# Performance work log

Hardware: AMD Instinct MI355X
Metric: run time of the kernel (lower is better)

Reference implementation:

```python
import jax, jax.numpy as jnp
import numpy as np

A, B, D = 64, 128, 256   # batch, route nodes, feature_dim
H, C = 64, 32            # hidden_capsule, center_num
NUM_ITERS = 3


def _squash(t, axis=-1):
    sq = jnp.sum(t * t, axis=axis, keepdims=True)
    return (sq / (1.0 + sq)) * t / jnp.sqrt(sq)


def _route(priors, n_iters):
    # priors: [K, A, R, D]; dynamic routing over axis=2 (R).
    # Original keeps logits of priors' full shape, but they stay constant
    # along D (init zeros, delta has keepdim on last axis), so [K,A,R,1]
    # is exactly equivalent and avoids a redundant [K,A,R,D] buffer.
    logits = jnp.zeros(priors.shape[:-1] + (1,), priors.dtype)
    outputs = None
    for i in range(n_iters):
        probs = jax.nn.softmax(logits, axis=2)          # [K,A,R,1]
        outputs = _squash(jnp.sum(probs * priors, axis=2, keepdims=True))  # [K,A,1,D]
        if i != n_iters - 1:
            logits = logits + jnp.sum(priors * outputs, axis=-1, keepdims=True)
    return outputs


def setup_inputs() -> dict:
    key = jax.random.key(0)
    k1, k2, k3 = jax.random.split(key, 3)
    x = jax.random.normal(k1, (A, B, D), dtype=jnp.float32)
    route_weights1 = jax.random.normal(k2, (H, D, D), dtype=jnp.float32)
    route_weights = jax.random.normal(k3, (C, D, D), dtype=jnp.float32)
    return {"x": x, "route_weights1": route_weights1, "route_weights": route_weights}


def reference(x, route_weights1, route_weights):
    # stage 1: priors1[h,a,b,:] = x[a,b,:] @ W1[h]  -> [H,A,B,D]
    priors1 = jnp.einsum('abd,hde->habe', x, route_weights1)
    out1 = _route(priors1, NUM_ITERS)                  # [H,A,1,D]
    out1 = jnp.transpose(out1[:, :, 0, :], (1, 0, 2))  # squeeze + transpose(0,1) -> [A,H,D]
    # stage 2: priors[c,a,h,:] = out1[a,h,:] @ W[c]   -> [C,A,H,D]
    priors = jnp.einsum('ahd,cde->cahe', out1, route_weights)
    out = _route(priors, NUM_ITERS)                    # [C,A,1,D]
    return out[:, :, 0, :]                             # squeeze -> [C,A,D]
```

## Files before the change

kernel.cpp:

```cpp
#include <hip/hip_runtime.h>
#include <hip/hip_bf16.h>

typedef __attribute__((ext_vector_type(8))) short bf16x8;
typedef __attribute__((ext_vector_type(4))) float f32x4;
typedef unsigned short u16;
typedef unsigned int u32;

__device__ __forceinline__ u32 bf16_rne(float f) {
  u32 u = __float_as_uint(f);
  return (u + 0x7FFFu + ((u >> 16) & 1u)) >> 16;
}
__device__ __forceinline__ float bf16_val(u32 b) { return __uint_as_float(b << 16); }

__device__ __forceinline__ void g2l16(const u16* g, u16* l) {
  __builtin_amdgcn_global_load_lds(
      (const __attribute__((address_space(1))) u32*)g,
      (__attribute__((address_space(3))) u32*)l, 16, 0, 0);
}

__global__ void split_arr(const float* __restrict__ in,
                          u16* __restrict__ hi, u16* __restrict__ lo, int n4) {
  int i = blockIdx.x * 256 + threadIdx.x;
  if (i >= n4) return;
  float4 v = ((const float4*)in)[i];
  u32 h0 = bf16_rne(v.x), h1 = bf16_rne(v.y), h2 = bf16_rne(v.z), h3 = bf16_rne(v.w);
  u32 l0 = bf16_rne(v.x - bf16_val(h0));
  u32 l1 = bf16_rne(v.y - bf16_val(h1));
  u32 l2 = bf16_rne(v.z - bf16_val(h2));
  u32 l3 = bf16_rne(v.w - bf16_val(h3));
  ushort4 hv; hv.x = (u16)h0; hv.y = (u16)h1; hv.z = (u16)h2; hv.w = (u16)h3;
  ushort4 lv; lv.x = (u16)l0; lv.y = (u16)l1; lv.z = (u16)l2; lv.w = (u16)l3;
  ((ushort4*)hi)[i] = hv;
  ((ushort4*)lo)[i] = lv;
}

__global__ void split_transpose256(const float* __restrict__ in,
                                   u16* __restrict__ hi, u16* __restrict__ lo) {
  __shared__ float tile[32][33];
  const size_t off = (size_t)blockIdx.z * 65536;
  const int tx = threadIdx.x, ty = threadIdx.y;
#pragma unroll
  for (int i = 0; i < 4; ++i) {
    int y = blockIdx.y * 32 + ty + i * 8;
    int x = blockIdx.x * 32 + tx;
    tile[ty + i * 8][tx] = in[off + (size_t)y * 256 + x];
  }
  __syncthreads();
#pragma unroll
  for (int i = 0; i < 4; ++i) {
    float v = tile[tx][ty + i * 8];
    u32 hb = bf16_rne(v);
    u32 lb = bf16_rne(v - bf16_val(hb));
    size_t idx = off + (size_t)(blockIdx.x * 32 + ty + i * 8) * 256 + blockIdx.y * 32 + tx;
    hi[idx] = (u16)hb;
    lo[idx] = (u16)lb;
  }
}

template <int R>
__global__ __launch_bounds__(512, 4) void caps_route(
    const u16* __restrict__ Ahi_g,
    const u16* __restrict__ Alo_g,
    const u16* __restrict__ Whi,
    const u16* __restrict__ Wlo,
    u16* __restrict__ o1hi, u16* __restrict__ o1lo,
    float* __restrict__ outp,
    int KN, int stage) {
  constexpr int MTW = R / 32;
  constexpr int NA = R / 16;
  constexpr int NTOT = 2 * NA + 32;
  __shared__ u16 BUF[NTOT * 512];
  __shared__ __align__(16) float smat[2][256];
  __shared__ __align__(16) float wlog[4][R];
  __shared__ float logits[R];
  __shared__ __align__(16) float probs[R];
  __shared__ float sqpart[4];

  u16* Ahi = BUF;
  u16* Alo = BUF + NA * 512;
  u16* Bhi = BUF + 2 * NA * 512;
  u16* Blo = BUF + 2 * NA * 512 + 8192;

  const int tid = threadIdx.x;
  const int w = tid >> 6, lane = tid & 63, q = lane >> 4, li = lane & 15;
  const int mg = w >> 2, eg = w & 3;
  const int kk = blockIdx.x >> 6;
  const int a  = blockIdx.x & 63;

  const u16* ArH = Ahi_g + (size_t)a * R * 256;
  const u16* ArL = Alo_g + (size_t)a * R * 256;
  const u16* WhR = Whi + (size_t)kk * 65536;
  const u16* WlR = Wlo + (size_t)kk * 65536;

  f32x4 acc[MTW][4] = {};

  const int sub = lane >> 2, p = lane & 3;
  const int laneoff = sub * 256 + p * 8;

  for (int ks = 0; ks < 8; ++ks) {
    const int k0 = ks * 32;
#pragma unroll
    for (int c = w; c < NTOT; c += 8) {
      const u16* g;
      if (c < NA)              g = ArH + (c) * 4096;
      else if (c < 2 * NA)     g = ArL + (c - NA) * 4096;
      else if (c < 2 * NA + 16) g = WhR + (c - 2 * NA) * 4096;
      else                     g = WlR + (c - 2 * NA - 16) * 4096;
      g2l16(g + laneoff + k0, BUF + c * 512 + lane * 8);
    }
    __syncthreads();
    bf16x8 bh[4], bl[4];
#pragma unroll
    for (int ct = 0; ct < 4; ++ct) {
      int e = eg * 64 + ct * 16 + li;
      bh[ct] = *(const bf16x8*)(Bhi + e * 32 + q * 8);
      bl[ct] = *(const bf16x8*)(Blo + e * 32 + q * 8);
    }
#pragma unroll
    for (int mt = 0; mt < MTW; ++mt) {
      int row = mg * (R / 2) + mt * 16 + li;
      bf16x8 ah = *(const bf16x8*)(Ahi + row * 32 + q * 8);
      bf16x8 al = *(const bf16x8*)(Alo + row * 32 + q * 8);
#pragma unroll
      for (int ct = 0; ct < 4; ++ct) {
        acc[mt][ct] = __builtin_amdgcn_mfma_f32_16x16x32_bf16(al, bh[ct], acc[mt][ct], 0, 0, 0);
        acc[mt][ct] = __builtin_amdgcn_mfma_f32_16x16x32_bf16(ah, bl[ct], acc[mt][ct], 0, 0, 0);
        acc[mt][ct] = __builtin_amdgcn_mfma_f32_16x16x32_bf16(ah, bh[ct], acc[mt][ct], 0, 0, 0);
      }
    }
    __syncthreads();
  }

  const float invR = 1.0f / R;
  float v[4];

  for (int iter = 0; iter < 3; ++iter) {
    float sp[4];
#pragma unroll
    for (int ct = 0; ct < 4; ++ct) {
      float t = 0.f;
#pragma unroll
      for (int mt = 0; mt < MTW; ++mt) {
        float4 p4;
        if (iter == 0) { p4.x = invR; p4.y = invR; p4.z = invR; p4.w = invR; }
        else           { p4 = *(const float4*)&probs[mg * (R / 2) + mt * 16 + q * 4]; }
        t += p4.x * acc[mt][ct][0];
        t += p4.y * acc[mt][ct][1];
        t += p4.z * acc[mt][ct][2];
        t += p4.w * acc[mt][ct][3];
      }
      t += __shfl_xor(t, 16);
      t += __shfl_xor(t, 32);
      sp[ct] = t;
    }
    if (q == 0) {
#pragma unroll
      for (int ct = 0; ct < 4; ++ct) smat[mg][eg * 64 + ct * 16 + li] = sp[ct];
    }
    __syncthreads();
    float s[4];
#pragma unroll
    for (int ct = 0; ct < 4; ++ct) {
      int e = eg * 64 + ct * 16 + li;
      s[ct] = smat[0][e] + smat[1][e];
    }
    float ss = s[0] * s[0] + s[1] * s[1] + s[2] * s[2] + s[3] * s[3];
    ss += __shfl_xor(ss, 1);
    ss += __shfl_xor(ss, 2);
    ss += __shfl_xor(ss, 4);
    ss += __shfl_xor(ss, 8);
    if (mg == 0 && lane == 0) sqpart[eg] = ss;
    __syncthreads();
    float sq = sqpart[0] + sqpart[1] + sqpart[2] + sqpart[3];
    float scale = (sq > 0.f) ? sq / ((1.0f + sq) * sqrtf(sq)) : 0.f;
#pragma unroll
    for (int ct = 0; ct < 4; ++ct) v[ct] = s[ct] * scale;

    if (iter < 2) {
#pragma unroll
      for (int mt = 0; mt < MTW; ++mt) {
        float t0, t1, t2, t3;
        {
          float t = acc[mt][0][0] * v[0] + acc[mt][1][0] * v[1] +
                    acc[mt][2][0] * v[2] + acc[mt][3][0] * v[3];
          t += __shfl_xor(t, 1); t += __shfl_xor(t, 2);
          t += __shfl_xor(t, 4); t += __shfl_xor(t, 8);
          t0 = t;
        }
        {
          float t = acc[mt][0][1] * v[0] + acc[mt][1][1] * v[1] +
                    acc[mt][2][1] * v[2] + acc[mt][3][1] * v[3];
          t += __shfl_xor(t, 1); t += __shfl_xor(t, 2);
          t += __shfl_xor(t, 4); t += __shfl_xor(t, 8);
          t1 = t;
        }
        {
          float t = acc[mt][0][2] * v[0] + acc[mt][1][2] * v[1] +
                    acc[mt][2][2] * v[2] + acc[mt][3][2] * v[3];
          t += __shfl_xor(t, 1); t += __shfl_xor(t, 2);
          t += __shfl_xor(t, 4); t += __shfl_xor(t, 8);
          t2 = t;
        }
        {
          float t = acc[mt][0][3] * v[0] + acc[mt][1][3] * v[1] +
                    acc[mt][2][3] * v[2] + acc[mt][3][3] * v[3];
          t += __shfl_xor(t, 1); t += __shfl_xor(t, 2);
          t += __shfl_xor(t, 4); t += __shfl_xor(t, 8);
          t3 = t;
        }
        if (li == 0)
          *(float4*)&wlog[eg][mg * (R / 2) + mt * 16 + q * 4] = make_float4(t0, t1, t2, t3);
      }
      __syncthreads();
      if (tid < R) {
        float l = (iter == 0 ? 0.f : logits[tid]);
        l += wlog[0][tid] + wlog[1][tid] + wlog[2][tid] + wlog[3][tid];
        logits[tid] = l;
      }
      __syncthreads();
      if (w == 0) {
        float l0 = logits[lane];
        float l1 = (R == 128) ? logits[lane + 64] : -3.0e38f;
        float m = fmaxf(l0, l1);
#pragma unroll
        for (int d2 = 1; d2 < 64; d2 <<= 1) m = fmaxf(m, __shfl_xor(m, d2));
        float e0 = expf(l0 - m);
        float e1 = (R == 128) ? expf(l1 - m) : 0.f;
        float zz = e0 + e1;
#pragma unroll
        for (int d2 = 1; d2 < 64; d2 <<= 1) zz += __shfl_xor(zz, d2);
        float inv = 1.0f / zz;
        probs[lane] = e0 * inv;
        if (R == 128) probs[lane + 64] = e1 * inv;
      }
      __syncthreads();
    }
  }

  if (mg == 0 && q == 0) {
    if (stage == 1) {
      size_t ob = ((size_t)a * KN + kk) * 256;
#pragma unroll
      for (int ct = 0; ct < 4; ++ct) {
        int e = eg * 64 + ct * 16 + li;
        u32 hb = bf16_rne(v[ct]);
        u32 lb = bf16_rne(v[ct] - bf16_val(hb));
        o1hi[ob + e] = (u16)hb;
        o1lo[ob + e] = (u16)lb;
      }
    } else {
      size_t ob = ((size_t)kk * 64 + a) * 256;
#pragma unroll
      for (int ct = 0; ct < 4; ++ct) {
        int e = eg * 64 + ct * 16 + li;
        outp[ob + e] = v[ct];
      }
    }
  }
}

extern "C" void kernel_launch(void* const* d_in, const int* in_sizes, int n_in,
                              void* d_out, int out_size, void* d_ws, size_t ws_size,
                              hipStream_t stream) {
  const float* x  = (const float*)d_in[0];
  const float* w1 = (const float*)d_in[1];
  const float* wc = (const float*)d_in[2];
  float* out = (float*)d_out;

  char* ws = (char*)d_ws;
  u16* w1hi = (u16*)(ws);
  u16* w1lo = (u16*)(ws + (8u << 20));
  u16* wchi = (u16*)(ws + (16u << 20));
  u16* wclo = (u16*)(ws + (20u << 20));
  u16* xhi  = (u16*)(ws + (24u << 20));
  u16* xlo  = (u16*)(ws + (28u << 20));
  u16* o1hi = (u16*)(ws + (32u << 20));
  u16* o1lo = (u16*)(ws + (34u << 20));

  split_arr<<<2048, 256, 0, stream>>>(x, xhi, xlo, 524288);
  split_transpose256<<<dim3(8, 8, 64), dim3(32, 8), 0, stream>>>(w1, w1hi, w1lo);
  split_transpose256<<<dim3(8, 8, 32), dim3(32, 8), 0, stream>>>(wc, wchi, wclo);
  caps_route<128><<<64 * 64, 512, 0, stream>>>(xhi, xlo, w1hi, w1lo, o1hi, o1lo, nullptr, 64, 1);
  caps_route<64><<<32 * 64, 512, 0, stream>>>(o1hi, o1lo, wchi, wclo, nullptr, nullptr, out, 32, 2);
}
```

Measured before the change: 407.3 us.

## Interleave hi/lo bf16 splits per batch row and restructure LDS fragment layout

Stores the hi and lo bf16 halves of x, W1, Wc and stage-1 outputs contiguously per batch row or weight slab, so each block reads from one base pointer. The LDS staging now fills each 512-element chunk with a 16-row x 32-k fragment in MFMA-operand order, and each wave loads a fixed contiguous set of chunks, which replaces the branchy per-chunk pointer selection. The goal is simpler address arithmetic, better global locality, and conflict-free contiguous LDS fragment reads. The global access pattern changes, since 16 lanes now stride by rows, so coalescing may differ.

```diff
diff --git a/kernel.cpp b/kernel.cpp
--- a/kernel.cpp
+++ b/kernel.cpp
@@ -18,8 +18,8 @@
       (__attribute__((address_space(3))) u32*)l, 16, 0, 0);
 }
 
-__global__ void split_arr(const float* __restrict__ in,
-                          u16* __restrict__ hi, u16* __restrict__ lo, int n4) {
+__global__ void split_pairs(const float* __restrict__ in, u16* __restrict__ out,
+                            int n4, int chunk4) {
   int i = blockIdx.x * 256 + threadIdx.x;
   if (i >= n4) return;
   float4 v = ((const float4*)in)[i];
@@ -30,20 +30,21 @@
   u32 l3 = bf16_rne(v.w - bf16_val(h3));
   ushort4 hv; hv.x = (u16)h0; hv.y = (u16)h1; hv.z = (u16)h2; hv.w = (u16)h3;
   ushort4 lv; lv.x = (u16)l0; lv.y = (u16)l1; lv.z = (u16)l2; lv.w = (u16)l3;
-  ((ushort4*)hi)[i] = hv;
-  ((ushort4*)lo)[i] = lv;
-}
-
-__global__ void split_transpose256(const float* __restrict__ in,
-                                   u16* __restrict__ hi, u16* __restrict__ lo) {
+  int blk = i / chunk4, off = i % chunk4;
+  ((ushort4*)out)[(size_t)blk * 2 * chunk4 + off] = hv;
+  ((ushort4*)out)[(size_t)blk * 2 * chunk4 + chunk4 + off] = lv;
+}
+
+__global__ void split_transpose256(const float* __restrict__ in, u16* __restrict__ out) {
   __shared__ float tile[32][33];
-  const size_t off = (size_t)blockIdx.z * 65536;
+  const size_t zin = (size_t)blockIdx.z * 65536;
+  const size_t zout = (size_t)blockIdx.z * 131072;
   const int tx = threadIdx.x, ty = threadIdx.y;
 #pragma unroll
   for (int i = 0; i < 4; ++i) {
     int y = blockIdx.y * 32 + ty + i * 8;
     int x = blockIdx.x * 32 + tx;
-    tile[ty + i * 8][tx] = in[off + (size_t)y * 256 + x];
+    tile[ty + i * 8][tx] = in[zin + (size_t)y * 256 + x];
   }
   __syncthreads();
 #pragma unroll
@@ -51,76 +52,63 @@
     float v = tile[tx][ty + i * 8];
     u32 hb = bf16_rne(v);
     u32 lb = bf16_rne(v - bf16_val(hb));
-    size_t idx = off + (size_t)(blockIdx.x * 32 + ty + i * 8) * 256 + blockIdx.y * 32 + tx;
-    hi[idx] = (u16)hb;
-    lo[idx] = (u16)lb;
+    size_t idx = (size_t)(blockIdx.x * 32 + ty + i * 8) * 256 + blockIdx.y * 32 + tx;
+    out[zout + idx] = (u16)hb;
+    out[zout + 65536 + idx] = (u16)lb;
   }
 }
 
 template <int R>
 __global__ __launch_bounds__(512, 4) void caps_route(
-    const u16* __restrict__ Ahi_g,
-    const u16* __restrict__ Alo_g,
-    const u16* __restrict__ Whi,
-    const u16* __restrict__ Wlo,
-    u16* __restrict__ o1hi, u16* __restrict__ o1lo,
+    const u16* __restrict__ Ain,
+    const u16* __restrict__ Win,
+    u16* __restrict__ o1,
     float* __restrict__ outp,
     int KN, int stage) {
   constexpr int MTW = R / 32;
   constexpr int NA = R / 16;
   constexpr int NTOT = 2 * NA + 32;
-  __shared__ u16 BUF[NTOT * 512];
+  constexpr int CPW = NTOT / 8;
+  __shared__ __align__(16) u16 BUF[NTOT * 512];
   __shared__ __align__(16) float smat[2][256];
   __shared__ __align__(16) float wlog[4][R];
   __shared__ float logits[R];
   __shared__ __align__(16) float probs[R];
   __shared__ float sqpart[4];
 
-  u16* Ahi = BUF;
-  u16* Alo = BUF + NA * 512;
-  u16* Bhi = BUF + 2 * NA * 512;
-  u16* Blo = BUF + 2 * NA * 512 + 8192;
-
   const int tid = threadIdx.x;
   const int w = tid >> 6, lane = tid & 63, q = lane >> 4, li = lane & 15;
   const int mg = w >> 2, eg = w & 3;
   const int kk = blockIdx.x >> 6;
   const int a  = blockIdx.x & 63;
 
-  const u16* ArH = Ahi_g + (size_t)a * R * 256;
-  const u16* ArL = Alo_g + (size_t)a * R * 256;
-  const u16* WhR = Whi + (size_t)kk * 65536;
-  const u16* WlR = Wlo + (size_t)kk * 65536;
+  const u16* Aab = Ain + (size_t)a * 2 * R * 256;
+  const u16* Wkk = Win + (size_t)kk * 131072;
 
   f32x4 acc[MTW][4] = {};
 
-  const int sub = lane >> 2, p = lane & 3;
-  const int laneoff = sub * 256 + p * 8;
+  const int laneoff = (lane & 15) * 256 + (lane >> 4) * 8;
+  const int fo = (q * 16 + li) * 8;
 
   for (int ks = 0; ks < 8; ++ks) {
     const int k0 = ks * 32;
 #pragma unroll
-    for (int c = w; c < NTOT; c += 8) {
-      const u16* g;
-      if (c < NA)              g = ArH + (c) * 4096;
-      else if (c < 2 * NA)     g = ArL + (c - NA) * 4096;
-      else if (c < 2 * NA + 16) g = WhR + (c - 2 * NA) * 4096;
-      else                     g = WlR + (c - 2 * NA - 16) * 4096;
-      g2l16(g + laneoff + k0, BUF + c * 512 + lane * 8);
+    for (int j = 0; j < CPW; ++j) {
+      int c = w * CPW + j;
+      const u16* g = (c < 2 * NA) ? (Aab + c * 4096) : (Wkk + (c - 2 * NA) * 4096);
+      g2l16(g + laneoff + k0, BUF + c * 512);
     }
     __syncthreads();
     bf16x8 bh[4], bl[4];
 #pragma unroll
     for (int ct = 0; ct < 4; ++ct) {
-      int e = eg * 64 + ct * 16 + li;
-      bh[ct] = *(const bf16x8*)(Bhi + e * 32 + q * 8);
-      bl[ct] = *(const bf16x8*)(Blo + e * 32 + q * 8);
+      bh[ct] = *(const bf16x8*)(BUF + (2 * NA + eg * 4 + ct) * 512 + fo);
+      bl[ct] = *(const bf16x8*)(BUF + (2 * NA + 16 + eg * 4 + ct) * 512 + fo);
     }
 #pragma unroll
     for (int mt = 0; mt < MTW; ++mt) {
-      int row = mg * (R / 2) + mt * 16 + li;
-      bf16x8 ah = *(const bf16x8*)(Ahi + row * 32 + q * 8);
-      bf16x8 al = *(const bf16x8*)(Alo + row * 32 + q * 8);
+      bf16x8 ah = *(const bf16x8*)(BUF + (mg * MTW + mt) * 512 + fo);
+      bf16x8 al = *(const bf16x8*)(BUF + (NA + mg * MTW + mt) * 512 + fo);
 #pragma unroll
       for (int ct = 0; ct < 4; ++ct) {
         acc[mt][ct] = __builtin_amdgcn_mfma_f32_16x16x32_bf16(al, bh[ct], acc[mt][ct], 0, 0, 0);
@@ -239,14 +227,14 @@
 
   if (mg == 0 && q == 0) {
     if (stage == 1) {
-      size_t ob = ((size_t)a * KN + kk) * 256;
+      size_t ob = (size_t)a * 2 * KN * 256 + (size_t)kk * 256;
 #pragma unroll
       for (int ct = 0; ct < 4; ++ct) {
         int e = eg * 64 + ct * 16 + li;
         u32 hb = bf16_rne(v[ct]);
         u32 lb = bf16_rne(v[ct] - bf16_val(hb));
-        o1hi[ob + e] = (u16)hb;
-        o1lo[ob + e] = (u16)lb;
+        o1[ob + e] = (u16)hb;
+        o1[ob + (size_t)KN * 256 + e] = (u16)lb;
       }
     } else {
       size_t ob = ((size_t)kk * 64 + a) * 256;
@@ -268,18 +256,14 @@
   float* out = (float*)d_out;
 
   char* ws = (char*)d_ws;
-  u16* w1hi = (u16*)(ws);
-  u16* w1lo = (u16*)(ws + (8u << 20));
-  u16* wchi = (u16*)(ws + (16u << 20));
-  u16* wclo = (u16*)(ws + (20u << 20));
-  u16* xhi  = (u16*)(ws + (24u << 20));
-  u16* xlo  = (u16*)(ws + (28u << 20));
-  u16* o1hi = (u16*)(ws + (32u << 20));
-  u16* o1lo = (u16*)(ws + (34u << 20));
-
-  split_arr<<<2048, 256, 0, stream>>>(x, xhi, xlo, 524288);
-  split_transpose256<<<dim3(8, 8, 64), dim3(32, 8), 0, stream>>>(w1, w1hi, w1lo);
-  split_transpose256<<<dim3(8, 8, 32), dim3(32, 8), 0, stream>>>(wc, wchi, wclo);
-  caps_route<128><<<64 * 64, 512, 0, stream>>>(xhi, xlo, w1hi, w1lo, o1hi, o1lo, nullptr, 64, 1);
-  caps_route<64><<<32 * 64, 512, 0, stream>>>(o1hi, o1lo, wchi, wclo, nullptr, nullptr, out, 32, 2);
-}
+  u16* x2  = (u16*)(ws);
+  u16* w12 = (u16*)(ws + (16u << 20));
+  u16* wc2 = (u16*)(ws + (32u << 20));
+  u16* o1  = (u16*)(ws + (40u << 20));
+
+  split_pairs<<<2048, 256, 0, stream>>>(x, x2, 524288, 8192);
+  split_transpose256<<<dim3(8, 8, 64), dim3(32, 8), 0, stream>>>(w1, w12);
+  split_transpose256<<<dim3(8, 8, 32), dim3(32, 8), 0, stream>>>(wc, wc2);
+  caps_route<128><<<64 * 64, 512, 0, stream>>>(x2, w12, o1, nullptr, 64, 1);
+  caps_route<64><<<32 * 64, 512, 0, stream>>>(o1, wc2, nullptr, out, 32, 2);
+}
```

After: 425.0 us. 1.04x slower.
